# Performance work log

Hardware: AMD Instinct MI355X
Metric: run time of the kernel (lower is better)

The kernel has to match this reference:

```python
import jax, jax.numpy as jnp
import numpy as np

N = 50000      # nodes
E = 800000     # edges
IN = 128       # in_dim
OUT = 128      # out_dim
R = 4          # num_relations
H = 8          # heads
D = OUT // H   # per-head dim
NEG_SLOPE = 0.2


def setup_inputs() -> dict:
    key = jax.random.key(0)
    ks = jax.random.split(key, 12)
    s = 0.05
    return {
        "node_inp": jax.random.normal(ks[0], (N, IN), dtype=jnp.float32),
        "edge_index": jax.random.randint(ks[1], (2, E), 0, N),
        "edge_type": jax.random.randint(ks[2], (E,), 0, R),
        # per-relation GATConv params
        "W_rel": jax.random.normal(ks[3], (R, IN, OUT), dtype=jnp.float32) * s,
        "att_src_rel": jax.random.normal(ks[4], (R, H, D), dtype=jnp.float32) * s,
        "att_dst_rel": jax.random.normal(ks[5], (R, H, D), dtype=jnp.float32) * s,
        "bias_rel": jax.random.normal(ks[6], (R, OUT), dtype=jnp.float32) * s,
        # linear layers
        "W_self": jax.random.normal(ks[7], (IN, OUT), dtype=jnp.float32) * s,   # lin_self
        "W_cross": jax.random.normal(ks[8], (OUT, OUT), dtype=jnp.float32) * s,  # lin_cross
        # lang_conv GAT params (lin_l is Bypass, so no weight matrix)
        "att_src_lang": jax.random.normal(ks[9], (H, D), dtype=jnp.float32) * s,
        "att_dst_lang": jax.random.normal(ks[10], (H, D), dtype=jnp.float32) * s,
        "bias_lang": jax.random.normal(ks[11], (OUT,), dtype=jnp.float32) * s,
    }


def _hgnn_forward(node_inp, edge_index, edge_type, W_rel, att_src_rel,
                  att_dst_rel, bias_rel, W_self, W_cross,
                  att_src_lang, att_dst_lang, bias_lang):
    src, dst = edge_index[0], edge_index[1]

    def rel_gat(W, a_s, a_d, b, mask):
        # standard PyG GATConv (single x, add_self_loops=False), restricted to
        # edges with this relation type via mask
        x = (node_inp @ W).reshape(N, H, D)                     # [N,H,D]
        es = jnp.einsum('nhd,hd->nh', x, a_s)
        ed = jnp.einsum('nhd,hd->nh', x, a_d)
        logit = jax.nn.leaky_relu(es[src] + ed[dst], NEG_SLOPE)  # [E,H]
        logit = jnp.where(mask[:, None], logit, -1e30)
        mx = jax.ops.segment_max(logit, dst, num_segments=N)     # [N,H]
        mx = jnp.maximum(mx, -1e30)                              # avoid -inf
        p = jnp.exp(logit - mx[dst]) * mask[:, None]
        den = jax.ops.segment_sum(p, dst, num_segments=N)        # [N,H]
        alpha = p / jnp.where(den > 0, den, 1.0)[dst]            # [E,H]
        msg = alpha[..., None] * x[src]                          # [E,H,D]
        out = jax.ops.segment_sum(msg, dst, num_segments=N)      # [N,H,D]
        tmask = jax.ops.segment_sum(mask.astype(jnp.float32), dst,
                                    num_segments=N) > 0          # [N] target nodes
        return out.reshape(N, OUT) + b, tmask

    rel_masks = edge_type[None, :] == jnp.arange(R)[:, None]     # [R,E]
    rel_out, tmask = jax.vmap(rel_gat)(W_rel, att_src_rel, att_dst_rel,
                                       bias_rel, rel_masks)      # [R,N,OUT],[R,N]
    h = jax.nn.gelu(rel_out, approximate=False) @ W_cross        # [R,N,OUT]

    S = node_inp @ W_self                                        # [N,OUT] self entries
    # lang_conv: per node i, GAT attention over entries {self(i)} U
    # {rel outputs at i for relations where i is a target}. lin_l = Bypass,
    # and since x is a single tensor in PyG, x_dst = rel_inputs[i] = S[i].
    ent = jnp.concatenate([S[None], h], axis=0).reshape(R + 1, N, H, D)
    valid = jnp.concatenate([jnp.ones((1, N), bool), tmask], axis=0)  # [R+1,N]
    ls = jnp.einsum('knhd,hd->knh', ent, att_src_lang)
    ld = jnp.einsum('nhd,hd->nh', ent[0], att_dst_lang)
    logit = jax.nn.leaky_relu(ls + ld[None], NEG_SLOPE)          # [R+1,N,H]
    logit = jnp.where(valid[..., None], logit, -jnp.inf)
    alpha = jax.nn.softmax(logit, axis=0)                        # self always valid
    out = jnp.einsum('knh,knhd->nhd', alpha, ent).reshape(N, OUT)
    return out + bias_lang


def reference(node_inp, edge_index, edge_type, W_rel, att_src_rel, att_dst_rel,
              bias_rel, W_self, W_cross, att_src_lang, att_dst_lang, bias_lang):
    return _hgnn_forward(node_inp, edge_index, edge_type, W_rel, att_src_rel,
                         att_dst_rel, bias_rel, W_self, W_cross,
                         att_src_lang, att_dst_lang, bias_lang)
```

## Files before the change

kernel.cpp:

```cpp
#include <hip/hip_runtime.h>
#include <hip/hip_bf16.h>
#include <math.h>

#define NN 50000
#define NE 800000
#define NREL 4
#define NHEAD 8
#define NSEG (NREL * NN)
#define BCAP 26

typedef __hip_bfloat16 bf16;
typedef short short8 __attribute__((ext_vector_type(8)));
typedef float floatx4 __attribute__((ext_vector_type(4)));

#define LOG2E 1.4426950408889634f

__device__ __forceinline__ float b2f(bf16 v) { return __bfloat162float(v); }
__device__ __forceinline__ float us2f(unsigned short u) {
    return __uint_as_float(((unsigned)u) << 16);
}
__device__ __forceinline__ unsigned short f2us(float v) {
    bf16 b = __float2bfloat16(v);
    return *(unsigned short*)&b;
}

__device__ __forceinline__ float gelu_f(float v) {
    float z = v * 0.70710678118654752f;
    float az = fabsf(z);
    float t = __builtin_amdgcn_rcpf(__builtin_fmaf(0.3275911f, az, 1.f));
    float p = t * (0.254829592f +
              t * (-0.284496736f +
              t * (1.421413741f +
              t * (-1.453152027f +
              t * 1.061405429f))));
    float ex = __builtin_amdgcn_exp2f(az * az * -LOG2E);
    float er = copysignf(1.f - p * ex, z);
    return 0.5f * v * (1.f + er);
}

__global__ void fill_kernel(float* __restrict__ out, int n) {
    int t = blockIdx.x * blockDim.x + threadIdx.x;
    if (t < n) out[t] = 1000.0f;
}

__global__ __launch_bounds__(256) void prep_scatter(
    const float* __restrict__ W_rel,
    const float* __restrict__ W_self,
    const float* __restrict__ W_cross,
    const float* __restrict__ a_src,
    const float* __restrict__ a_dst,
    const float* __restrict__ node_inp,
    const int* __restrict__ ei,
    const int* __restrict__ et,
    bf16* __restrict__ Wt, bf16* __restrict__ Wct,
    bf16* __restrict__ Ab,
    int* __restrict__ counts,
    unsigned short* __restrict__ bkt) {
    int t = blockIdx.x * blockDim.x + threadIdx.x;

    int src = 0, pos = BCAP;
    unsigned seg = 0;
    if (t < NE) {
        src = ei[t];
        int dst = ei[NE + t];
        seg = (unsigned)(et[t] * NN + dst);
        pos = atomicAdd(&counts[seg], 1);
    }

    if (t < 768 * 128) {
        int row = t >> 7, k = t & 127;
        float v;
        if (row < 512) {
            int r = row >> 7, c = row & 127;
            v = W_rel[(r * 128 + k) * 128 + c];
        } else if (row < 640) {
            v = W_self[k * 128 + (row - 512)];
        } else if (row < 704) {
            int q = row - 640;
            bool is_src = q < 32;
            int qq = is_src ? q : q - 32;
            int r = qq >> 3, h = qq & 7;
            const float* av = (is_src ? a_src : a_dst) + (r * 8 + h) * 16;
            const float* wr = W_rel + (size_t)(r * 128 + k) * 128 + h * 16;
            float s = 0.f;
            #pragma unroll
            for (int dd = 0; dd < 16; ++dd) s += wr[dd] * av[dd];
            v = s * LOG2E;
        } else {
            v = 0.f;
        }
        Wt[t] = __float2bfloat16(v);
    } else if (t < 768 * 128 + 128 * 128) {
        int u = t - 768 * 128;
        int n = u >> 7, k = u & 127;
        Wct[u] = __float2bfloat16(W_cross[k * 128 + n]);
    }

    if (t < NN * 16) {
        const float* ap = node_inp + (size_t)t * 8;
        float4 f0 = *(const float4*)ap;
        float4 f1 = *(const float4*)(ap + 4);
        short8 v = (short8){(short)f2us(f0.x), (short)f2us(f0.y),
                            (short)f2us(f0.z), (short)f2us(f0.w),
                            (short)f2us(f1.x), (short)f2us(f1.y),
                            (short)f2us(f1.z), (short)f2us(f1.w)};
        *(short8*)(Ab + (size_t)t * 8) = v;
    }

    if (t < NE && pos < BCAP)
        bkt[seg * (unsigned)BCAP + (unsigned)pos] = (unsigned short)src;
}

__global__ __launch_bounds__(256) void gemm_node(
    const bf16* __restrict__ Ab,
    const bf16* __restrict__ Bt,
    bf16* __restrict__ outb,
    float* __restrict__ outf,
    unsigned short* __restrict__ es_u,
    unsigned short* __restrict__ ed_u,
    int M)
{
    __shared__ __align__(16) char smem[25600];
    short (*As)[40] = (short (*)[40])smem;
    short (*Bs)[40] = (short (*)[40])(smem + 5120);

    const int tid  = threadIdx.x;
    const int wave = tid >> 6, lane = tid & 63;
    const int quad = lane >> 4, l16 = lane & 15;
    const int wr_ = wave & 1, wc = wave >> 1;
    const int row0 = blockIdx.x * 64;
    const int plane = blockIdx.y;
    const int col0 = plane * 256;

    floatx4 acc[2][8];
    #pragma unroll
    for (int i = 0; i < 2; ++i)
        #pragma unroll
        for (int j = 0; j < 8; ++j) acc[i][j] = (floatx4){0.f, 0.f, 0.f, 0.f};

    for (int k0 = 0; k0 < 128; k0 += 32) {
        {
            int c = tid;
            int r = c >> 2, off = (c & 3) * 8;
            int gr = row0 + r;
            short8 v = {0, 0, 0, 0, 0, 0, 0, 0};
            if (gr < M)
                v = *(const short8*)(Ab + (((size_t)gr) << 7) + k0 + off);
            *(short8*)&As[r][off] = v;
        }
        #pragma unroll
        for (int i = 0; i < 4; ++i) {
            int c = i * 256 + tid;
            int r = c >> 2, off = (c & 3) * 8;
            short8 w = *(const short8*)(Bt + (((size_t)(col0 + r)) << 7) + k0 + off);
            *(short8*)&Bs[r][off] = w;
        }
        __syncthreads();

        short8 av[2], bv[8];
        #pragma unroll
        for (int mt = 0; mt < 2; ++mt)
            av[mt] = *(const short8*)&As[wr_ * 32 + mt * 16 + l16][quad * 8];
        #pragma unroll
        for (int nt = 0; nt < 8; ++nt)
            bv[nt] = *(const short8*)&Bs[wc * 128 + nt * 16 + l16][quad * 8];
        #pragma unroll
        for (int mt = 0; mt < 2; ++mt)
            #pragma unroll
            for (int nt = 0; nt < 8; ++nt)
                acc[mt][nt] = __builtin_amdgcn_mfma_f32_16x16x32_bf16(
                    av[mt], bv[nt], acc[mt][nt], 0, 0, 0);
        __syncthreads();
    }

    const bool eswave = (plane == 2 && wc == 1);
    if (eswave) {
        #pragma unroll
        for (int mt = 0; mt < 2; ++mt) {
            #pragma unroll
            for (int reg = 0; reg < 4; ++reg) {
                int gr = row0 + wr_ * 32 + mt * 16 + quad * 4 + reg;
                if (gr >= M) continue;
                #pragma unroll
                for (int nt = 0; nt < 4; ++nt) {
                    int q = nt * 16 + l16;
                    unsigned short v = f2us(acc[mt][nt][reg]);
                    if (q < 32)
                        es_u[(unsigned)((q >> 3) * NN + gr) * 8u + (unsigned)(q & 7)] = v;
                    else
                        ed_u[(unsigned)(((q - 32) >> 3) * NN + gr) * 8u + (unsigned)((q - 32) & 7)] = v;
                }
            }
        }
    }

    float* ct = (float*)(smem + wave * 4352);
    const int rr2 = lane >> 2;
    const int cc0 = (lane & 3) * 16;

    for (int mt = 0; mt < 2; ++mt) {
        #pragma unroll
        for (int half = 0; half < 2; ++half) {
            if (!eswave) {
                #pragma unroll
                for (int nt = 0; nt < 4; ++nt)
                    #pragma unroll
                    for (int reg = 0; reg < 4; ++reg)
                        ct[(quad * 4 + reg) * 68 + nt * 16 + l16] =
                            acc[mt][half * 4 + nt][reg];
            }
            __syncthreads();
            if (!eswave) {
                int gr2 = row0 + wr_ * 32 + mt * 16 + rr2;
                if (gr2 < M) {
                    float4 f0 = *(const float4*)&ct[rr2 * 68 + cc0];
                    float4 f1 = *(const float4*)&ct[rr2 * 68 + cc0 + 4];
                    float4 f2 = *(const float4*)&ct[rr2 * 68 + cc0 + 8];
                    float4 f3 = *(const float4*)&ct[rr2 * 68 + cc0 + 12];
                    int lc = half * 64 + cc0;
                    if (plane == 2) {
                        float* dst = outf + (((size_t)gr2) << 7) + lc;
                        __builtin_nontemporal_store(*(const floatx4*)&f0, (floatx4*)dst);
                        __builtin_nontemporal_store(*(const floatx4*)&f1, (floatx4*)(dst + 4));
                        __builtin_nontemporal_store(*(const floatx4*)&f2, (floatx4*)(dst + 8));
                        __builtin_nontemporal_store(*(const floatx4*)&f3, (floatx4*)(dst + 12));
                    } else {
                        int rel = plane * 2 + wc;
                        float tmp[16] = {f0.x, f0.y, f0.z, f0.w, f1.x, f1.y, f1.z, f1.w,
                                         f2.x, f2.y, f2.z, f2.w, f3.x, f3.y, f3.z, f3.w};
                        short8 o0, o1;
                        #pragma unroll
                        for (int j = 0; j < 8; ++j) o0[j] = (short)f2us(tmp[j]);
                        #pragma unroll
                        for (int j = 0; j < 8; ++j) o1[j] = (short)f2us(tmp[8 + j]);
                        bf16* dst = outb + ((size_t)(rel * NN + gr2) << 7) + lc;
                        *(short8*)dst = o0;
                        *(short8*)(dst + 8) = o1;
                    }
                }
            }
            __syncthreads();
        }
    }
}

__global__ __launch_bounds__(256) void agg_kernel(
    const unsigned short* __restrict__ bkt, const int* __restrict__ counts,
    const bf16* __restrict__ Xb, const unsigned short* __restrict__ es_u,
    const unsigned short* __restrict__ ed_u, const float* __restrict__ bias_rel,
    bf16* __restrict__ Gb4, unsigned char* __restrict__ flag)
{
    const int rel  = blockIdx.y;
    const int wave = threadIdx.x >> 6, l = threadIdx.x & 63;
    const int n    = blockIdx.x * 16 + wave * 4 + (l >> 4);
    const int l16  = l & 15;
    const int f0   = l16 * 8;
    const int h    = l16 >> 1;

    const unsigned seg = (unsigned)(rel * NN + n);
    int cnt = counts[seg];
    cnt = cnt < BCAP ? cnt : BCAP;
    const unsigned short* bk  = bkt + seg * (unsigned)BCAP;
    const float edv = us2f(ed_u[seg * 8u + (unsigned)h]);
    const unsigned short* Xr  = (const unsigned short*)Xb +
                                (size_t)rel * (size_t)(NN * 128);
    const unsigned short* esr = es_u + (unsigned)rel * (unsigned)(NN * 8);

    float a[8];
    #pragma unroll
    for (int j = 0; j < 8; ++j) a[j] = 0.f;
    float den = 0.f;

    int e = 0;
    for (; e + 1 < cnt; e += 2) {
        unsigned pair = *(const unsigned*)(bk + e);
        int s0 = (int)(pair & 0xFFFFu);
        int s1 = (int)(pair >> 16);
        float e0 = us2f(esr[(unsigned)s0 * 8u + (unsigned)h]);
        float e1 = us2f(esr[(unsigned)s1 * 8u + (unsigned)h]);
        short8 u0 = *(const short8*)(Xr + (size_t)s0 * 128 + f0);
        short8 u1 = *(const short8*)(Xr + (size_t)s1 * 128 + f0);
        float aa0 = e0 + edv, aa1 = e1 + edv;
        float w0 = __builtin_amdgcn_exp2f(fmaxf(aa0, 0.2f * aa0));
        float w1 = __builtin_amdgcn_exp2f(fmaxf(aa1, 0.2f * aa1));
        #pragma unroll
        for (int j = 0; j < 8; ++j)
            a[j] += w0 * us2f((unsigned short)u0[j]) +
                    w1 * us2f((unsigned short)u1[j]);
        den += w0 + w1;
    }
    if (e < cnt) {
        int s0 = (int)bk[e];
        float e0 = us2f(esr[(unsigned)s0 * 8u + (unsigned)h]);
        short8 u0 = *(const short8*)(Xr + (size_t)s0 * 128 + f0);
        float aa0 = e0 + edv;
        float w0 = __builtin_amdgcn_exp2f(fmaxf(aa0, 0.2f * aa0));
        #pragma unroll
        for (int j = 0; j < 8; ++j) a[j] += w0 * us2f((unsigned short)u0[j]);
        den += w0;
    }

    float inv = den > 0.f ? __builtin_amdgcn_rcpf(den) : 0.f;
    const float* bp = bias_rel + rel * 128 + f0;
    float4 b0 = *(const float4*)bp;
    float4 b1 = *(const float4*)(bp + 4);
    float bb[8] = {b0.x, b0.y, b0.z, b0.w, b1.x, b1.y, b1.z, b1.w};
    short8 o;
    #pragma unroll
    for (int j = 0; j < 8; ++j)
        o[j] = (short)f2us(gelu_f(__builtin_fmaf(a[j], inv, bb[j])));
    __builtin_nontemporal_store(o, (short8*)((unsigned short*)Gb4 +
        ((size_t)((unsigned)n * 4u + (unsigned)rel)) * 128u + (unsigned)f0));
    if (l16 == 0)
        flag[(unsigned)n * 4u + (unsigned)rel] = (unsigned char)(cnt > 0);
}

__global__ __launch_bounds__(256) void gemm_lang(
    const bf16* __restrict__ A,
    const bf16* __restrict__ Bt,
    const unsigned char* __restrict__ flag,
    const float* __restrict__ asl_g,
    const float* __restrict__ adl_g,
    const float* __restrict__ bias_lang,
    float* __restrict__ out)
{
    __shared__ __align__(16) char smem[15360];
    short (*As)[40] = (short (*)[40])smem;
    short (*Bs)[40] = (short (*)[40])(smem + 5120);

    const int M = NN * NREL;
    const int tid  = threadIdx.x;
    const int wave = tid >> 6, lane = tid & 63;
    const int quad = lane >> 4, l16 = lane & 15;
    const int wr_ = wave & 1, wc = wave >> 1;
    const int row0 = blockIdx.x * 64;

    floatx4 acc[2][4];
    #pragma unroll
    for (int i = 0; i < 2; ++i)
        #pragma unroll
        for (int j = 0; j < 4; ++j) acc[i][j] = (floatx4){0.f, 0.f, 0.f, 0.f};

    for (int k0 = 0; k0 < 128; k0 += 32) {
        {
            int c = tid;
            int r = c >> 2, off = (c & 3) * 8;
            int gr = row0 + r;
            short8 v = {0, 0, 0, 0, 0, 0, 0, 0};
            if (gr < M)
                v = *(const short8*)(A + (((size_t)gr) << 7) + k0 + off);
            *(short8*)&As[r][off] = v;
        }
        #pragma unroll
        for (int i = 0; i < 2; ++i) {
            int c = tid * 2 + i;
            int r = c >> 2, off = (c & 3) * 8;
            short8 w = *(const short8*)(Bt + (((size_t)r) << 7) + k0 + off);
            *(short8*)&Bs[r][off] = w;
        }
        __syncthreads();

        short8 av[2], bv[4];
        #pragma unroll
        for (int mt = 0; mt < 2; ++mt)
            av[mt] = *(const short8*)&As[wr_ * 32 + mt * 16 + l16][quad * 8];
        #pragma unroll
        for (int nt = 0; nt < 4; ++nt)
            bv[nt] = *(const short8*)&Bs[wc * 64 + nt * 16 + l16][quad * 8];
        #pragma unroll
        for (int mt = 0; mt < 2; ++mt)
            #pragma unroll
            for (int nt = 0; nt < 4; ++nt)
                acc[mt][nt] = __builtin_amdgcn_mfma_f32_16x16x32_bf16(
                    av[mt], bv[nt], acc[mt][nt], 0, 0, 0);
        __syncthreads();
    }

    const int nb0 = blockIdx.x * 16 + wr_ * 8;
    #pragma unroll
    for (int nt = 0; nt < 4; ++nt) {
        int col = wc * 64 + nt * 16 + l16;
        float asl = asl_g[col];
        float adl = adl_g[col];
        float bl  = bias_lang[col];
        #pragma unroll
        for (int mt = 0; mt < 2; ++mt) {
            int node = nb0 + mt * 4 + quad;
            bool ok = node < NN;
            float Sv = ok ? out[(unsigned)node * 128u + (unsigned)col] : 0.f;
            float h0 = acc[mt][nt][0], h1 = acc[mt][nt][1];
            float h2 = acc[mt][nt][2], h3 = acc[mt][nt][3];
            float t0 = h0 * asl, t1 = h1 * asl, t2 = h2 * asl, t3 = h3 * asl;
            float ts = Sv * asl, td = Sv * adl;
            #pragma unroll
            for (int off = 1; off < 16; off <<= 1) {
                t0 += __shfl_xor(t0, off);
                t1 += __shfl_xor(t1, off);
                t2 += __shfl_xor(t2, off);
                t3 += __shfl_xor(t3, off);
                ts += __shfl_xor(ts, off);
                td += __shfl_xor(td, off);
            }
            unsigned fl = ok ? *(const unsigned*)(flag + (unsigned)node * 4u) : 0u;
            float aS = ts + td, a0 = t0 + td, a1 = t1 + td, a2 = t2 + td, a3 = t3 + td;
            float lS = fmaxf(aS, 0.2f * aS);
            float l0 = fmaxf(a0, 0.2f * a0);
            float l1 = fmaxf(a1, 0.2f * a1);
            float l2 = fmaxf(a2, 0.2f * a2);
            float l3 = fmaxf(a3, 0.2f * a3);
            bool v0 = (fl & 0x000000FFu) != 0, v1 = (fl & 0x0000FF00u) != 0;
            bool v2 = (fl & 0x00FF0000u) != 0, v3 = (fl & 0xFF000000u) != 0;
            float m = lS;
            if (v0) m = fmaxf(m, l0);
            if (v1) m = fmaxf(m, l1);
            if (v2) m = fmaxf(m, l2);
            if (v3) m = fmaxf(m, l3);
            float eS = __expf(lS - m);
            float e0 = v0 ? __expf(l0 - m) : 0.f;
            float e1 = v1 ? __expf(l1 - m) : 0.f;
            float e2 = v2 ? __expf(l2 - m) : 0.f;
            float e3 = v3 ? __expf(l3 - m) : 0.f;
            float sum = eS + e0 + e1 + e2 + e3;
            float o = eS * Sv + e0 * h0 + e1 * h1 + e2 * h2 + e3 * h3;
            o = o / sum + bl;
            if (ok) __builtin_nontemporal_store(o, &out[(unsigned)node * 128u + (unsigned)col]);
        }
    }
}

extern "C" void kernel_launch(void* const* d_in, const int* in_sizes, int n_in,
                              void* d_out, int out_size, void* d_ws, size_t ws_size,
                              hipStream_t stream) {
    const float* node_inp     = (const float*)d_in[0];
    const int*   edge_index   = (const int*)d_in[1];
    const int*   edge_type    = (const int*)d_in[2];
    const float* W_rel        = (const float*)d_in[3];
    const float* att_src_rel  = (const float*)d_in[4];
    const float* att_dst_rel  = (const float*)d_in[5];
    const float* bias_rel     = (const float*)d_in[6];
    const float* W_self       = (const float*)d_in[7];
    const float* W_cross      = (const float*)d_in[8];
    const float* att_src_lang = (const float*)d_in[9];
    const float* att_dst_lang = (const float*)d_in[10];
    const float* bias_lang    = (const float*)d_in[11];
    (void)in_sizes; (void)n_in;

    const size_t SZ_XB   = (size_t)NREL * NN * 128 * 2;
    const size_t SZ_ES   = (size_t)NREL * NN * 8 * 2;
    const size_t SZ_GB4  = (size_t)NREL * NN * 128 * 2;
    const size_t SZ_WT   = 768 * 128 * 2;
    const size_t SZ_WCT  = 128 * 128 * 2;
    const size_t SZ_BKT  = (size_t)NSEG * BCAP * 2;
    const size_t SZ_CNT  = (size_t)NSEG * 4;
    const size_t SZ_FLG  = (size_t)NN * 4;
    const size_t TOTAL = SZ_XB + 2 * SZ_ES + SZ_GB4 + SZ_WT + SZ_WCT +
                         SZ_BKT + SZ_CNT + SZ_FLG;

    if (ws_size < TOTAL) {
        fill_kernel<<<(out_size + 255) / 256, 256, 0, stream>>>((float*)d_out, out_size);
        return;
    }

    char* ws = (char*)d_ws;
    size_t o = 0;
    bf16*  Xb      = (bf16*)(ws + o);  o += SZ_XB;
    unsigned short* es_u = (unsigned short*)(ws + o); o += SZ_ES;
    unsigned short* ed_u = (unsigned short*)(ws + o); o += SZ_ES;
    bf16*  Gb4     = (bf16*)(ws + o);  o += SZ_GB4;
    bf16*  Wt      = (bf16*)(ws + o);  o += SZ_WT;
    bf16*  Wct     = (bf16*)(ws + o);  o += SZ_WCT;
    unsigned short* bkt = (unsigned short*)(ws + o); o += SZ_BKT;
    int*   counts  = (int*)(ws + o);   o += SZ_CNT;
    unsigned char* flag = (unsigned char*)(ws + o);
    float* S       = (float*)d_out;
    bf16*  Ab      = Gb4;

    hipMemsetAsync(counts, 0, SZ_CNT, stream);

    prep_scatter<<<(NE + 255) / 256, 256, 0, stream>>>(
        W_rel, W_self, W_cross, att_src_rel, att_dst_rel, node_inp,
        edge_index, edge_type, Wt, Wct, Ab, counts, bkt);

    dim3 g1((NN + 63) / 64, 3);
    gemm_node<<<g1, 256, 0, stream>>>(Ab, Wt, Xb, S, es_u, ed_u, NN);

    dim3 ga(NN / 16, NREL);
    agg_kernel<<<ga, 256, 0, stream>>>(bkt, counts, Xb, es_u, ed_u, bias_rel, Gb4, flag);

    dim3 g2((NREL * NN + 63) / 64, 1);
    gemm_lang<<<g2, 256, 0, stream>>>(Gb4, Wct, flag, att_src_lang, att_dst_lang,
                                      bias_lang, (float*)d_out);
}
```

Measured before the change: 282.6 us.

## Fold lang source attention into extra GEMM columns and prefetch self features

Extends the transposed W_cross with 16 extra columns holding W_cross·att_src_lang (scaled by log2e), so gemm_lang computes per-head source logits through MFMA rather than 4-way shuffle reductions per output. Logits are exchanged through LDS and exp switches to exp2. The self features and validity flags are loaded before the K loop to hide their latency. This costs an extra MFMA tile for half the waves, a larger LDS buffer and an extra barrier, and drops the node<NN bounds checks.

```diff
diff --git a/kernel.cpp b/kernel.cpp
--- a/kernel.cpp
+++ b/kernel.cpp
@@ -49,6 +49,7 @@
     const float* __restrict__ W_cross,
     const float* __restrict__ a_src,
     const float* __restrict__ a_dst,
+    const float* __restrict__ a_src_lang,
     const float* __restrict__ node_inp,
     const int* __restrict__ ei,
     const int* __restrict__ et,
@@ -90,10 +91,26 @@
             v = 0.f;
         }
         Wt[t] = __float2bfloat16(v);
-    } else if (t < 768 * 128 + 128 * 128) {
+    } else if (t < 768 * 128 + 144 * 128) {
         int u = t - 768 * 128;
         int n = u >> 7, k = u & 127;
-        Wct[u] = __float2bfloat16(W_cross[k * 128 + n]);
+        float v;
+        if (n < 128) {
+            v = W_cross[k * 128 + n];
+        } else {
+            int h = n - 128;
+            if (h < 8) {
+                const float* av = a_src_lang + h * 16;
+                const float* wr = W_cross + k * 128 + h * 16;
+                float s = 0.f;
+                #pragma unroll
+                for (int dd = 0; dd < 16; ++dd) s += wr[dd] * av[dd];
+                v = s * LOG2E;
+            } else {
+                v = 0.f;
+            }
+        }
+        Wct[u] = __float2bfloat16(v);
     }
 
     if (t < NN * 16) {
@@ -324,9 +341,10 @@
     const float* __restrict__ bias_lang,
     float* __restrict__ out)
 {
-    __shared__ __align__(16) char smem[15360];
+    __shared__ __align__(16) char smem[16640];
     short (*As)[40] = (short (*)[40])smem;
     short (*Bs)[40] = (short (*)[40])(smem + 5120);
+    float (*ls_lds)[4][9] = (float (*)[4][9])smem;
 
     const int M = NN * NREL;
     const int tid  = threadIdx.x;
@@ -334,12 +352,26 @@
     const int quad = lane >> 4, l16 = lane & 15;
     const int wr_ = wave & 1, wc = wave >> 1;
     const int row0 = blockIdx.x * 64;
-
-    floatx4 acc[2][4];
+    const int node0 = blockIdx.x * 16;
+
+    float svp[2][4];
+    unsigned flw[2];
+    #pragma unroll
+    for (int mt = 0; mt < 2; ++mt) {
+        int node = node0 + wr_ * 8 + mt * 4 + quad;
+        flw[mt] = *(const unsigned*)(flag + (unsigned)node * 4u);
+        #pragma unroll
+        for (int nt = 0; nt < 4; ++nt)
+            svp[mt][nt] = out[(unsigned)node * 128u + (unsigned)(wc * 64 + nt * 16 + l16)];
+    }
+
+    floatx4 acc[2][5];
     #pragma unroll
     for (int i = 0; i < 2; ++i)
         #pragma unroll
-        for (int j = 0; j < 4; ++j) acc[i][j] = (floatx4){0.f, 0.f, 0.f, 0.f};
+        for (int j = 0; j < 5; ++j) acc[i][j] = (floatx4){0.f, 0.f, 0.f, 0.f};
+
+    const int NT = 4 + wc;
 
     for (int k0 = 0; k0 < 128; k0 += 32) {
         {
@@ -352,62 +384,70 @@
             *(short8*)&As[r][off] = v;
         }
         #pragma unroll
-        for (int i = 0; i < 2; ++i) {
-            int c = tid * 2 + i;
-            int r = c >> 2, off = (c & 3) * 8;
-            short8 w = *(const short8*)(Bt + (((size_t)r) << 7) + k0 + off);
-            *(short8*)&Bs[r][off] = w;
+        for (int i = 0; i < 3; ++i) {
+            int c = i * 256 + tid;
+            if (c < 576) {
+                int r = c >> 2, off = (c & 3) * 8;
+                short8 w = *(const short8*)(Bt + (((size_t)r) << 7) + k0 + off);
+                *(short8*)&Bs[r][off] = w;
+            }
         }
         __syncthreads();
 
-        short8 av[2], bv[4];
+        short8 av[2], bv[5];
         #pragma unroll
         for (int mt = 0; mt < 2; ++mt)
             av[mt] = *(const short8*)&As[wr_ * 32 + mt * 16 + l16][quad * 8];
-        #pragma unroll
-        for (int nt = 0; nt < 4; ++nt)
+        for (int nt = 0; nt < NT; ++nt)
             bv[nt] = *(const short8*)&Bs[wc * 64 + nt * 16 + l16][quad * 8];
         #pragma unroll
         for (int mt = 0; mt < 2; ++mt)
-            #pragma unroll
-            for (int nt = 0; nt < 4; ++nt)
+            for (int nt = 0; nt < NT; ++nt)
                 acc[mt][nt] = __builtin_amdgcn_mfma_f32_16x16x32_bf16(
                     av[mt], bv[nt], acc[mt][nt], 0, 0, 0);
         __syncthreads();
     }
 
-    const int nb0 = blockIdx.x * 16 + wr_ * 8;
+    if (wc == 1 && l16 < 8) {
+        #pragma unroll
+        for (int mt = 0; mt < 2; ++mt) {
+            int nl = wr_ * 8 + mt * 4 + quad;
+            #pragma unroll
+            for (int reg = 0; reg < 4; ++reg)
+                ls_lds[nl][reg][l16] = acc[mt][4][reg];
+        }
+    }
+    __syncthreads();
+
     #pragma unroll
     for (int nt = 0; nt < 4; ++nt) {
         int col = wc * 64 + nt * 16 + l16;
-        float asl = asl_g[col];
-        float adl = adl_g[col];
-        float bl  = bias_lang[col];
+        float aslL = asl_g[col] * LOG2E;
+        float adlL = adl_g[col] * LOG2E;
+        float bl   = bias_lang[col];
+        int hh = wc * 4 + nt;
         #pragma unroll
         for (int mt = 0; mt < 2; ++mt) {
-            int node = nb0 + mt * 4 + quad;
-            bool ok = node < NN;
-            float Sv = ok ? out[(unsigned)node * 128u + (unsigned)col] : 0.f;
-            float h0 = acc[mt][nt][0], h1 = acc[mt][nt][1];
-            float h2 = acc[mt][nt][2], h3 = acc[mt][nt][3];
-            float t0 = h0 * asl, t1 = h1 * asl, t2 = h2 * asl, t3 = h3 * asl;
-            float ts = Sv * asl, td = Sv * adl;
+            int nl = wr_ * 8 + mt * 4 + quad;
+            int node = node0 + nl;
+            float Sv = svp[mt][nt];
+            float ts = Sv * aslL, td = Sv * adlL;
             #pragma unroll
             for (int off = 1; off < 16; off <<= 1) {
-                t0 += __shfl_xor(t0, off);
-                t1 += __shfl_xor(t1, off);
-                t2 += __shfl_xor(t2, off);
-                t3 += __shfl_xor(t3, off);
                 ts += __shfl_xor(ts, off);
                 td += __shfl_xor(td, off);
             }
-            unsigned fl = ok ? *(const unsigned*)(flag + (unsigned)node * 4u) : 0u;
-            float aS = ts + td, a0 = t0 + td, a1 = t1 + td, a2 = t2 + td, a3 = t3 + td;
+            float g0 = ls_lds[nl][0][hh] + td;
+            float g1 = ls_lds[nl][1][hh] + td;
+            float g2 = ls_lds[nl][2][hh] + td;
+            float g3 = ls_lds[nl][3][hh] + td;
+            float aS = ts + td;
             float lS = fmaxf(aS, 0.2f * aS);
-            float l0 = fmaxf(a0, 0.2f * a0);
-            float l1 = fmaxf(a1, 0.2f * a1);
-            float l2 = fmaxf(a2, 0.2f * a2);
-            float l3 = fmaxf(a3, 0.2f * a3);
+            float l0 = fmaxf(g0, 0.2f * g0);
+            float l1 = fmaxf(g1, 0.2f * g1);
+            float l2 = fmaxf(g2, 0.2f * g2);
+            float l3 = fmaxf(g3, 0.2f * g3);
+            unsigned fl = flw[mt];
             bool v0 = (fl & 0x000000FFu) != 0, v1 = (fl & 0x0000FF00u) != 0;
             bool v2 = (fl & 0x00FF0000u) != 0, v3 = (fl & 0xFF000000u) != 0;
             float m = lS;
@@ -415,15 +455,16 @@
             if (v1) m = fmaxf(m, l1);
             if (v2) m = fmaxf(m, l2);
             if (v3) m = fmaxf(m, l3);
-            float eS = __expf(lS - m);
-            float e0 = v0 ? __expf(l0 - m) : 0.f;
-            float e1 = v1 ? __expf(l1 - m) : 0.f;
-            float e2 = v2 ? __expf(l2 - m) : 0.f;
-            float e3 = v3 ? __expf(l3 - m) : 0.f;
+            float eS = __builtin_amdgcn_exp2f(lS - m);
+            float e0 = v0 ? __builtin_amdgcn_exp2f(l0 - m) : 0.f;
+            float e1 = v1 ? __builtin_amdgcn_exp2f(l1 - m) : 0.f;
+            float e2 = v2 ? __builtin_amdgcn_exp2f(l2 - m) : 0.f;
+            float e3 = v3 ? __builtin_amdgcn_exp2f(l3 - m) : 0.f;
             float sum = eS + e0 + e1 + e2 + e3;
-            float o = eS * Sv + e0 * h0 + e1 * h1 + e2 * h2 + e3 * h3;
+            float o = eS * Sv + e0 * acc[mt][nt][0] + e1 * acc[mt][nt][1] +
+                      e2 * acc[mt][nt][2] + e3 * acc[mt][nt][3];
             o = o / sum + bl;
-            if (ok) __builtin_nontemporal_store(o, &out[(unsigned)node * 128u + (unsigned)col]);
+            __builtin_nontemporal_store(o, &out[(unsigned)node * 128u + (unsigned)col]);
         }
     }
 }
@@ -449,7 +490,7 @@
     const size_t SZ_ES   = (size_t)NREL * NN * 8 * 2;
     const size_t SZ_GB4  = (size_t)NREL * NN * 128 * 2;
     const size_t SZ_WT   = 768 * 128 * 2;
-    const size_t SZ_WCT  = 128 * 128 * 2;
+    const size_t SZ_WCT  = 144 * 128 * 2;
     const size_t SZ_BKT  = (size_t)NSEG * BCAP * 2;
     const size_t SZ_CNT  = (size_t)NSEG * 4;
     const size_t SZ_FLG  = (size_t)NN * 4;
@@ -478,8 +519,8 @@
     hipMemsetAsync(counts, 0, SZ_CNT, stream);
 
     prep_scatter<<<(NE + 255) / 256, 256, 0, stream>>>(
-        W_rel, W_self, W_cross, att_src_rel, att_dst_rel, node_inp,
-        edge_index, edge_type, Wt, Wct, Ab, counts, bkt);
+        W_rel, W_self, W_cross, att_src_rel, att_dst_rel, att_src_lang,
+        node_inp, edge_index, edge_type, Wt, Wct, Ab, counts, bkt);
 
     dim3 g1((NN + 63) / 64, 3);
     gemm_node<<<g1, 256, 0, stream>>>(Ab, Wt, Xb, S, es_u, ed_u, NN);
```

Result: slower. 1.081 ms (+282.5%).
